# Optimization experiments

Measured on AMD Instinct MI355X. Metric: run time of the kernel, lower is better.

The kernel has to match this reference:

```python
import jax, jax.numpy as jnp
import numpy as np

LN_EPS = 1e-5
REG_STRENGTH = 0.01  # torchsort soft_rank regularization_strength


def layer_norm(x, g, b):
    mu = jnp.mean(x, axis=-1, keepdims=True)
    var = jnp.var(x, axis=-1, keepdims=True)
    return (x - mu) * jax.lax.rsqrt(var + LN_EPS) * g + b


def pava_blocks(y):
    """Block ids of the non-increasing isotonic regression of y (PAVA).
    Returns int32 [n]: index of the block each position belongs to."""
    n = y.shape[0]

    def step(carry, yi):
        sums, counts, size = carry
        sums = sums.at[size].set(yi)
        counts = counts.at[size].set(1)
        size = size + 1

        def cond(st):
            s_, c_, sz = st
            m_prev = s_[sz - 2] / jnp.maximum(c_[sz - 2], 1).astype(s_.dtype)
            m_top = s_[sz - 1] / jnp.maximum(c_[sz - 1], 1).astype(s_.dtype)
            return (sz >= 2) & (m_prev <= m_top)

        def body(st):
            s_, c_, sz = st
            s_ = s_.at[sz - 2].add(s_[sz - 1])
            c_ = c_.at[sz - 2].add(c_[sz - 1])
            return s_, c_, sz - 1

        sums, counts, size = jax.lax.while_loop(cond, body, (sums, counts, size))
        return (sums, counts, size), None

    init = (jnp.zeros(n, y.dtype), jnp.zeros(n, jnp.int32), jnp.int32(0))
    (sums, counts, size), _ = jax.lax.scan(step, init, y)
    # expand block index over positions; trailing counts are 0 so total == n
    return jnp.repeat(jnp.arange(n, dtype=jnp.int32), counts, total_repeat_length=n)


def isotonic_l2_noninc(y):
    """argmin_{v1>=v2>=...>=vn} ||v - y||^2 via PAVA; block structure is
    computed on stop_gradient(y), solution is a differentiable segment mean."""
    n = y.shape[0]
    bid = pava_blocks(jax.lax.stop_gradient(y))
    bsum = jax.ops.segment_sum(y, bid, num_segments=n)
    bcnt = jax.ops.segment_sum(jnp.ones_like(y), bid, num_segments=n)
    return (bsum / jnp.maximum(bcnt, 1.0))[bid]


def soft_rank_row(scores):
    """torchsort.soft_rank(regularization='l2') on one row [n]."""
    n = scores.shape[0]
    theta = scores / REG_STRENGTH
    perm = jax.lax.stop_gradient(jnp.argsort(-theta))  # descending sort perm
    s = theta[perm]
    w = jnp.arange(n, 0, -1, dtype=scores.dtype)  # [n, n-1, ..., 1]
    dual = isotonic_l2_noninc(s - w)
    primal = s - dual
    return jnp.zeros(n, scores.dtype).at[perm].set(primal)


def setup_inputs() -> dict:
    key = jax.random.key(0)
    ks = jax.random.split(key, 3)
    B, rows, feat, hid = 32, 16384, 256, 16
    return {
        "table": jax.random.normal(ks[0], (B, rows, feat), dtype=jnp.float32),
        "ln1_g": jnp.ones((feat,), jnp.float32),
        "ln1_b": jnp.zeros((feat,), jnp.float32),
        "W1": 0.02 * jax.random.normal(ks[1], (feat, hid), dtype=jnp.float32),
        "b1": jnp.zeros((hid,), jnp.float32),
        "ln2_g": jnp.ones((hid,), jnp.float32),
        "ln2_b": jnp.zeros((hid,), jnp.float32),
        "W2": 0.02 * jax.random.normal(ks[2], (hid, 1), dtype=jnp.float32),
        "b2": jnp.zeros((1,), jnp.float32),
        "capacity": 64,
    }


def reference(table, ln1_g, ln1_b, W1, b1, ln2_g, ln2_b, W2, b2, capacity):
    B, rows, feat = table.shape
    h = layer_norm(table, ln1_g, ln1_b)
    h = jax.nn.relu(jnp.einsum('brf,fh->brh', h, W1) + b1)
    h = layer_norm(h, ln2_g, ln2_b)
    scores = (jnp.einsum('brh,ho->bro', h, W2) + b2)[..., 0]  # [B, rows]
    mn = jnp.min(scores, axis=1, keepdims=True)
    mx = jnp.max(scores, axis=1, keepdims=True)
    scaled = (scores - mn) / (mx - mn) * 100.0
    soft_ranks = jax.vmap(soft_rank_row)(scaled)  # [B, rows]
    hard_ranks = jnp.argsort(jnp.argsort(scores, axis=1), axis=1)  # inverse perm
    bins = hard_ranks // capacity + 1
    return soft_ranks[..., None], bins[..., None]
```

## Files before the change

### kernel.cpp

```cpp
#include <hip/hip_runtime.h>

#define NB 32
#define NR 16384
#define NF 256
#define NH 16
#define TOT (NB*NR)
#define RPB 256
#define KC 32
#define LSTR 33
#define SEGP 16386

typedef unsigned long long u64;

__device__ __forceinline__ unsigned int f2u(float f) {
    unsigned int u = __float_as_uint(f);
    return (u & 0x80000000u) ? ~u : (u | 0x80000000u);
}
__device__ __forceinline__ float u2f(unsigned int s) {
    unsigned int u = (s & 0x80000000u) ? (s ^ 0x80000000u) : ~s;
    return __uint_as_float(u);
}

__global__ __launch_bounds__(256) void k_prep(
    const float* __restrict__ ln1_g, const float* __restrict__ ln1_b,
    const float* __restrict__ W1, const float* __restrict__ b1,
    const float* __restrict__ ln2_g, const float* __restrict__ ln2_b,
    const float* __restrict__ W2, const float* __restrict__ b2,
    float* __restrict__ W1g, float* __restrict__ consts,
    unsigned* __restrict__ mnmx)
{
    __shared__ float redc[16][16];
    __shared__ float redu[16][16];
    const int t = threadIdx.x;
    for (int e = t; e < NF*NH; e += 256) {
        int k = e >> 4;
        W1g[e] = ln1_g[k] * W1[e];
    }
    if (t < NB) { mnmx[2*t] = 0u; mnmx[2*t + 1] = 0xFFFFFFFFu; }
    const int h = t & 15, kp = t >> 4;
    float pc = 0.f, pu = 0.f;
    #pragma unroll
    for (int r = 0; r < 16; ++r) {
        int k = kp*16 + r;
        float w = W1[k*NH + h];
        pc += ln1_b[k] * w;
        pu += ln1_g[k] * w;
    }
    redc[kp][h] = pc; redu[kp][h] = pu;
    __syncthreads();
    if (t < 16) {
        float sc = 0.f, su = 0.f;
        #pragma unroll
        for (int r = 0; r < 16; ++r) { sc += redc[r][t]; su += redu[r][t]; }
        consts[t]      = sc + b1[t];
        consts[16 + t] = su;
        consts[32 + t] = ln2_g[t] * W2[t];
    }
    if (t == 0) {
        float U2 = 0.f, C2 = b2[0];
        for (int hh = 0; hh < 16; ++hh) {
            U2 += ln2_g[hh] * W2[hh];
            C2 += ln2_b[hh] * W2[hh];
        }
        consts[48] = U2;
        consts[49] = C2;
    }
}

__global__ __launch_bounds__(256) void k_scores(
    const float* __restrict__ table,
    const float* __restrict__ W1g,
    const float* __restrict__ consts,
    u64* __restrict__ keys, unsigned* __restrict__ mnmx)
{
    __shared__ float xt[RPB * LSTR];
    __shared__ unsigned redmx[4], redmn[4];
    const int t = threadIdx.x;
    const size_t rowBase = (size_t)blockIdx.x * RPB;
    const int bb = blockIdx.x >> 6;
    const float4* __restrict__ Wg4 = (const float4*)W1g;

    float dx[16];
    #pragma unroll
    for (int h = 0; h < 16; ++h) dx[h] = 0.f;
    float sum = 0.f, ssq = 0.f;

    for (int c = 0; c < NF/KC; ++c) {
        float4 v[8];
        #pragma unroll
        for (int p = 0; p < 8; ++p) {
            int q = p*256 + t;
            int r = q >> 3, cg = q & 7;
            v[p] = *(const float4*)(table + (rowBase + r)*NF + c*KC + cg*4);
        }
        __syncthreads();
        #pragma unroll
        for (int p = 0; p < 8; ++p) {
            int q = p*256 + t;
            int r = q >> 3, cg = q & 7;
            float* dst = xt + r*LSTR + cg*4;
            dst[0] = v[p].x; dst[1] = v[p].y; dst[2] = v[p].z; dst[3] = v[p].w;
        }
        __syncthreads();

        const float* __restrict__ xr = xt + t*LSTR;
        #pragma unroll 4
        for (int k = 0; k < KC; ++k) {
            const int kk = c*KC + k;
            float x = xr[k];
            float4 w0 = Wg4[kk*4+0];
            float4 w1 = Wg4[kk*4+1];
            float4 w2 = Wg4[kk*4+2];
            float4 w3 = Wg4[kk*4+3];
            sum += x;
            ssq = fmaf(x, x, ssq);
            dx[ 0] = fmaf(x, w0.x, dx[ 0]);
            dx[ 1] = fmaf(x, w0.y, dx[ 1]);
            dx[ 2] = fmaf(x, w0.z, dx[ 2]);
            dx[ 3] = fmaf(x, w0.w, dx[ 3]);
            dx[ 4] = fmaf(x, w1.x, dx[ 4]);
            dx[ 5] = fmaf(x, w1.y, dx[ 5]);
            dx[ 6] = fmaf(x, w1.z, dx[ 6]);
            dx[ 7] = fmaf(x, w1.w, dx[ 7]);
            dx[ 8] = fmaf(x, w2.x, dx[ 8]);
            dx[ 9] = fmaf(x, w2.y, dx[ 9]);
            dx[10] = fmaf(x, w2.z, dx[10]);
            dx[11] = fmaf(x, w2.w, dx[11]);
            dx[12] = fmaf(x, w3.x, dx[12]);
            dx[13] = fmaf(x, w3.y, dx[13]);
            dx[14] = fmaf(x, w3.z, dx[14]);
            dx[15] = fmaf(x, w3.w, dx[15]);
        }
    }

    const float mu   = sum * (1.f/NF);
    const float var  = ssq * (1.f/NF) - mu*mu;
    const float rstd = rsqrtf(var + 1e-5f);
    float s2 = 0.f, q2 = 0.f, dh = 0.f;
    #pragma unroll
    for (int h = 0; h < 16; ++h) {
        float hv = rstd * (dx[h] - mu * consts[16 + h]) + consts[h];
        hv = fmaxf(hv, 0.f);
        s2 += hv;
        q2 = fmaf(hv, hv, q2);
        dh = fmaf(hv, consts[32 + h], dh);
    }
    const float mu2   = s2 * (1.f/NH);
    const float var2  = q2 * (1.f/NH) - mu2*mu2;
    const float rstd2 = rsqrtf(var2 + 1e-5f);
    const float sc    = rstd2 * (dh - mu2 * consts[48]) + consts[49];

    const size_t row = rowBase + t;
    const unsigned k32 = f2u(sc);
    keys[row] = ((u64)k32 << 32) | (u64)(row & (NR-1));

    unsigned wmx = k32, wmn = k32;
    #pragma unroll
    for (int m = 32; m >= 1; m >>= 1) {
        wmx = max(wmx, (unsigned)__shfl_xor((int)wmx, m, 64));
        wmn = min(wmn, (unsigned)__shfl_xor((int)wmn, m, 64));
    }
    const int lane = t & 63, wid = t >> 6;
    if (lane == 0) { redmx[wid] = wmx; redmn[wid] = wmn; }
    __syncthreads();
    if (t == 0) {
        unsigned bx = redmx[0], bn = redmn[0];
        #pragma unroll
        for (int w = 1; w < 4; ++w) { bx = max(bx, redmx[w]); bn = min(bn, redmn[w]); }
        atomicMax(&mnmx[2*bb], bx);
        atomicMin(&mnmx[2*bb + 1], bn);
    }
}

__global__ __launch_bounds__(1024) void k_sort_local(u64* __restrict__ keys) {
    __shared__ u64 sk[4096];
    const int base_g = blockIdx.x * 4096;
    const int tid = threadIdx.x;
    #pragma unroll
    for (int it = 0; it < 4; ++it) sk[tid + it*1024] = keys[base_g + tid + it*1024];
    __syncthreads();
    for (int k = 2; k <= 4096; k <<= 1) {
        for (int j = k >> 1; j > 0; j >>= 1) {
            int ii[2]; u64 a[2], c[2];
            #pragma unroll
            for (int it = 0; it < 2; ++it) {
                int q = tid + it*1024;
                int i = ((q & ~(j-1)) << 1) | (q & (j-1));
                ii[it] = i;
                a[it] = sk[i]; c[it] = sk[i | j];
            }
            #pragma unroll
            for (int it = 0; it < 2; ++it) {
                int gi = (base_g + ii[it]) & (NR - 1);
                bool dir = ((gi & k) == 0);
                if ((c[it] > a[it]) == dir) { sk[ii[it]] = c[it]; sk[ii[it] | j] = a[it]; }
            }
            __syncthreads();
        }
    }
    #pragma unroll
    for (int it = 0; it < 4; ++it) keys[base_g + tid + it*1024] = sk[tid + it*1024];
}

__global__ __launch_bounds__(1024) void k_mtail(u64* __restrict__ keys, int K) {
    __shared__ u64 sk[4096];
    const int base_g = blockIdx.x * 4096;
    const int tid = threadIdx.x;
    #pragma unroll
    for (int it = 0; it < 4; ++it) sk[tid + it*1024] = keys[base_g + tid + it*1024];
    const bool dir = (((base_g & (NR-1)) & K) == 0);
    __syncthreads();
    for (int j = 2048; j >= 1; j >>= 1) {
        int ii[2]; u64 a[2], c[2];
        #pragma unroll
        for (int it = 0; it < 2; ++it) {
            int q = tid + it*1024;
            int i = ((q & ~(j-1)) << 1) | (q & (j-1));
            ii[it] = i;
            a[it] = sk[i]; c[it] = sk[i | j];
        }
        #pragma unroll
        for (int it = 0; it < 2; ++it) {
            if ((c[it] > a[it]) == dir) { sk[ii[it]] = c[it]; sk[ii[it] | j] = a[it]; }
        }
        __syncthreads();
    }
    #pragma unroll
    for (int it = 0; it < 4; ++it) keys[base_g + tid + it*1024] = sk[tid + it*1024];
}

__global__ __launch_bounds__(256) void k_gpass(u64* __restrict__ keys, int k, int j) {
    int gt = blockIdx.x * 256 + threadIdx.x;
    int b  = gt >> 13;
    int t  = gt & 8191;
    int i  = ((t & ~(j-1)) << 1) | (t & (j-1));
    bool dir = ((i & k) == 0);
    u64* kb = keys + (size_t)b * NR;
    u64 a = kb[i], c = kb[i | j];
    if ((c > a) == dir) { kb[i] = c; kb[i | j] = a; }
}

__global__ __launch_bounds__(1024) void k_hullA(
    u64* __restrict__ keys, const unsigned* __restrict__ mnmx,
    int* __restrict__ Hg, double* __restrict__ Svg,
    int* __restrict__ cntg, double* __restrict__ sumg)
{
    __shared__ __align__(16) char smem[32768 + 16384 + 128 + 1024 + 3*512];
    u64*    sk  = (u64*)smem;
    double* S   = (double*)smem;
    int*    H   = (int*)(smem + 32768);
    double* Wt  = (double*)(smem + 32768 + 16384);
    int*    cnt = (int*)(smem + 32768 + 16384 + 128);
    int*    ti  = (int*)(smem + 32768 + 16384 + 128 + 1024);
    int*    tj  = (int*)(smem + 32768 + 16384 + 128 + 1024 + 512);
    int*    crA = (int*)(smem + 32768 + 16384 + 128 + 1024 + 1024);

    const int blk = blockIdx.x;
    const int b = blk >> 2, c = blk & 3;
    const int tid = threadIdx.x, lane = tid & 63, wid = tid >> 6;
    u64* kg = keys + (size_t)b * NR + c * 4096;

    #pragma unroll
    for (int it = 0; it < 4; ++it) sk[tid + it*1024] = kg[tid + it*1024];
    __syncthreads();
    for (int j = 2048; j >= 1; j >>= 1) {
        int ii[2]; u64 a[2], cc[2];
        #pragma unroll
        for (int it = 0; it < 2; ++it) {
            int q = tid + it*1024;
            int i = ((q & ~(j-1)) << 1) | (q & (j-1));
            ii[it] = i;
            a[it] = sk[i]; cc[it] = sk[i | j];
        }
        #pragma unroll
        for (int it = 0; it < 2; ++it) {
            if (cc[it] > a[it]) { sk[ii[it]] = cc[it]; sk[ii[it] | j] = a[it]; }
        }
        __syncthreads();
    }

    const float mx = u2f(mnmx[2*b]);
    const float mn = u2f(mnmx[2*b + 1]);
    const float scale = 10000.0f / (mx - mn);
    const int gofs = c * 4096;
    const int b4 = tid * 4;

    u64 kv[4];
    #pragma unroll
    for (int r = 0; r < 4; ++r) kv[r] = sk[b4 + r];
    #pragma unroll
    for (int it = 0; it < 4; ++it) kg[tid + it*1024] = sk[tid + it*1024];

    double loc[4];
    double acc = 0.0;
    #pragma unroll
    for (int r = 0; r < 4; ++r) {
        int ig = gofs + b4 + r;
        float s_i = (u2f((unsigned)(kv[r] >> 32)) - mn) * scale;
        acc += (double)s_i - (double)(NR - ig);
        loc[r] = acc;
    }
    __syncthreads();

    double v = acc;
    #pragma unroll
    for (int d = 1; d < 64; d <<= 1) {
        double o = __shfl_up(v, d, 64);
        if (lane >= d) v += o;
    }
    if (lane == 63) Wt[wid] = v;
    __syncthreads();
    if (tid < 16) {
        double w = Wt[tid];
        #pragma unroll
        for (int d = 1; d < 16; d <<= 1) {
            double o = __shfl_up(w, d, 16);
            if ((tid & 15) >= d) w += o;
        }
        Wt[tid] = w;
    }
    __syncthreads();
    const double wbase = (wid == 0) ? 0.0 : Wt[wid - 1];
    const double excl = wbase + (v - acc);
    #pragma unroll
    for (int r = 0; r < 4; ++r) S[b4 + r] = excl + loc[r];
    __syncthreads();
    if (tid == 0) sumg[blk] = S[4095];

    #define SVA(k) ((k) == 0 ? 0.0 : S[(k)-1])

    if (tid < 256) {
        const int base16 = tid * 16;
        int out = 0;
        int k1 = 0, k2 = 0; double y1 = 0.0, y2 = 0.0;
        #pragma unroll 1
        for (int r = 0; r < 16; ++r) {
            int k = base16 + r;
            double yk = SVA(k);
            while (out >= 2) {
                double cr_ = (double)(k1 - k2)*(yk - y2) - (y1 - y2)*(double)(k - k2);
                if (cr_ >= 0.0) {
                    --out; k1 = k2; y1 = y2;
                    if (out >= 2) { k2 = H[base16 + out - 2]; y2 = SVA(k2); }
                } else break;
            }
            H[base16 + out] = k;
            k2 = k1; y2 = y1; k1 = k; y1 = yk;
            ++out;
        }
        cnt[tid] = out;
    }

    for (int lev = 0; lev < 8; ++lev) {
        __syncthreads();
        const int pairs = 128 >> lev;
        const int Wd = 16 << lev;
        if (tid < pairs) {
            const int lbase = tid * 2 * Wd;
            const int rbase = lbase + Wd;
            int cl = cnt[(2*tid) << lev];
            int cr = cnt[(2*tid+1) << lev];
            int i = cl - 1, j = 0;
            int kLi = H[lbase + i];            double yLi = SVA(kLi);
            int kLm = 0;                       double yLm = 0.0;
            if (i > 0) { kLm = H[lbase + i - 1]; yLm = SVA(kLm); }
            int kRj = H[rbase];                double yRj = SVA(kRj);
            int kRn = 0;                       double yRn = 0.0;
            if (cr > 1) { kRn = H[rbase + 1]; yRn = SVA(kRn); }
            bool moved = true;
            while (moved) {
                moved = false;
                while (i > 0) {
                    double cr_ = (double)(kLi - kLm)*(yRj - yLm)
                               - (yLi - yLm)*(double)(kRj - kLm);
                    if (cr_ >= 0.0) {
                        --i; kLi = kLm; yLi = yLm;
                        if (i > 0) { kLm = H[lbase + i - 1]; yLm = SVA(kLm); }
                        moved = true;
                    } else break;
                }
                while (j < cr - 1) {
                    double cr_ = (double)(kRj - kLi)*(yRn - yLi)
                               - (yRj - yLi)*(double)(kRn - kLi);
                    if (cr_ >= 0.0) {
                        ++j; kRj = kRn; yRj = yRn;
                        if (j < cr - 1) { kRn = H[rbase + j + 1]; yRn = SVA(kRn); }
                        moved = true;
                    } else break;
                }
            }
            ti[tid] = i; tj[tid] = j; crA[tid] = cr;
            cnt[(2*tid) << lev] = (i + 1) + (cr - j);
        }
        __syncthreads();
        const int tpp = 8 << lev;
        const int p = tid / tpp;
        const int q = tid % tpp;
        int vals[8];
        int len = 0, srcb = 0, dstb = 0;
        if (p < pairs) {
            const int lbase = p * 2 * Wd;
            const int rbase = lbase + Wd;
            const int i = ti[p], j = tj[p], cr = crA[p];
            len = cr - j;
            srcb = rbase + j;
            dstb = lbase + i + 1;
            #pragma unroll
            for (int t2 = 0; t2 < 8; ++t2) {
                int e2 = q + t2 * tpp;
                if (e2 < len) vals[t2] = H[srcb + e2];
            }
        }
        __syncthreads();
        if (p < pairs) {
            #pragma unroll
            for (int t2 = 0; t2 < 8; ++t2) {
                int e2 = q + t2 * tpp;
                if (e2 < len) H[dstb + e2] = vals[t2];
            }
        }
        __syncthreads();
    }

    const int m = cnt[0];
    for (int p = tid; p < m; p += 1024) {
        int k = H[p];
        Hg[(size_t)blk * 4096 + p]  = k + gofs;
        Svg[(size_t)blk * 4096 + p] = SVA(k);
    }
    if (tid == 0) cntg[blk] = m;
    #undef SVA
}

__global__ __launch_bounds__(1024) void k_hullB(
    const double* __restrict__ sumg,
    int* __restrict__ Hg, double* __restrict__ Svg,
    const int* __restrict__ cntg,
    int* __restrict__ segk, float* __restrict__ segs, int* __restrict__ mseg)
{
    __shared__ int cnt[4];
    __shared__ int tiS[2], tjS[2], crS[2];
    __shared__ double beta[5];
    const int b = blockIdx.x;
    const int tid = threadIdx.x;
    int*    Hb = Hg  + (size_t)b * NR;
    double* Sb = Svg + (size_t)b * NR;

    if (tid < 4) cnt[tid] = cntg[4*b + tid];
    if (tid == 0) {
        double s = 0.0;
        #pragma unroll
        for (int c = 0; c < 4; ++c) { beta[c] = s; s += sumg[4*b + c]; }
        beta[4] = s;
    }
    __syncthreads();

    #pragma unroll 1
    for (int c = 0; c < 4; ++c) {
        const double bc = beta[c];
        for (int p = tid; p < cnt[c]; p += 1024) Sb[c*4096 + p] += bc;
    }
    __syncthreads();

    for (int lev = 0; lev < 2; ++lev) {
        const int pairs = 2 >> lev;
        const int Wd = 4096 << lev;
        if (tid < pairs) {
            const int lbase = tid * 2 * Wd;
            const int rbase = lbase + Wd;
            int cl = cnt[(2*tid) << lev];
            int cr = cnt[(2*tid+1) << lev];
            int i = cl - 1, j = 0;
            int kLi = Hb[lbase + i];            double yLi = Sb[lbase + i];
            int kLm = 0;                        double yLm = 0.0;
            if (i > 0) { kLm = Hb[lbase + i - 1]; yLm = Sb[lbase + i - 1]; }
            int kRj = Hb[rbase];                double yRj = Sb[rbase];
            int kRn = 0;                        double yRn = 0.0;
            if (cr > 1) { kRn = Hb[rbase + 1]; yRn = Sb[rbase + 1]; }
            bool moved = true;
            while (moved) {
                moved = false;
                while (i > 0) {
                    double cr_ = (double)(kLi - kLm)*(yRj - yLm)
                               - (yLi - yLm)*(double)(kRj - kLm);
                    if (cr_ >= 0.0) {
                        --i; kLi = kLm; yLi = yLm;
                        if (i > 0) { kLm = Hb[lbase + i - 1]; yLm = Sb[lbase + i - 1]; }
                        moved = true;
                    } else break;
                }
                while (j < cr - 1) {
                    double cr_ = (double)(kRj - kLi)*(yRn - yLi)
                               - (yRj - yLi)*(double)(kRn - kLi);
                    if (cr_ >= 0.0) {
                        ++j; kRj = kRn; yRj = yRn;
                        if (j < cr - 1) { kRn = Hb[rbase + j + 1]; yRn = Sb[rbase + j + 1]; }
                        moved = true;
                    } else break;
                }
            }
            tiS[tid] = i; tjS[tid] = j; crS[tid] = cr;
            cnt[(2*tid) << lev] = (i + 1) + (cr - j);
        }
        __syncthreads();
        const int tpp = (lev == 0) ? 512 : 1024;
        const int p = tid / tpp;
        const int q = tid % tpp;
        int hv[8]; double sv[8];
        int len = 0, srcb = 0, dstb = 0;
        if (p < pairs) {
            const int lbase = p * 2 * Wd;
            const int rbase = lbase + Wd;
            const int i = tiS[p], j = tjS[p], cr = crS[p];
            len = cr - j;
            srcb = rbase + j;
            dstb = lbase + i + 1;
            #pragma unroll
            for (int t2 = 0; t2 < 8; ++t2) {
                int e2 = q + t2 * tpp;
                if (e2 < len) { hv[t2] = Hb[srcb + e2]; sv[t2] = Sb[srcb + e2]; }
            }
        }
        __syncthreads();
        if (p < pairs) {
            #pragma unroll
            for (int t2 = 0; t2 < 8; ++t2) {
                int e2 = q + t2 * tpp;
                if (e2 < len) { Hb[dstb + e2] = hv[t2]; Sb[dstb + e2] = sv[t2]; }
            }
        }
        __syncthreads();
    }

    if (tid == 0) {
        const double total = beta[4];
        int out = cnt[0];
        while (out >= 2) {
            int ka = Hb[out - 2], kb2 = Hb[out - 1];
            double ya = Sb[out - 2], yb = Sb[out - 1];
            double cr_ = (double)(kb2 - ka)*(total - ya) - (yb - ya)*(double)(NR - ka);
            if (cr_ >= 0.0) --out;
            else break;
        }
        Hb[out] = NR; Sb[out] = total;
        cnt[0] = out + 1;
    }
    __syncthreads();

    const int m = cnt[0];
    for (int p = tid; p < m - 1; p += 1024) {
        int ka = Hb[p], kb2 = Hb[p + 1];
        segk[(size_t)b * SEGP + p] = ka;
        segs[(size_t)b * SEGP + p] = (float)((Sb[p + 1] - Sb[p]) / (double)(kb2 - ka));
    }
    if (tid == 0) mseg[b] = m;
}

__global__ __launch_bounds__(256) void k_out(
    const u64* __restrict__ keys, const unsigned* __restrict__ mnmx,
    const int* __restrict__ capp,
    const int* __restrict__ segk, const float* __restrict__ segs,
    const int* __restrict__ mseg,
    float* __restrict__ out_soft, float* __restrict__ out_bins)
{
    const int gb = blockIdx.x;
    const int b = gb >> 4, part = gb & 15;
    const int tid = threadIdx.x;
    const int m = mseg[b];
    const float mx = u2f(mnmx[2*b]);
    const float mn = u2f(mnmx[2*b + 1]);
    const float scale = 10000.0f / (mx - mn);
    const int cap = capp[0];
    const int base = part * 1024;
    const int* __restrict__ sk2 = segk + (size_t)b * SEGP;
    const float* __restrict__ ss2 = segs + (size_t)b * SEGP;

    int lo[4], hi[4];
    #pragma unroll
    for (int r = 0; r < 4; ++r) { lo[r] = 0; hi[r] = m - 1; }
    for (int step = 0; step < 14; ++step) {
        int hm[4];
        #pragma unroll
        for (int r = 0; r < 4; ++r)
            if (hi[r] - lo[r] > 1) hm[r] = sk2[(lo[r] + hi[r]) >> 1];
        #pragma unroll
        for (int r = 0; r < 4; ++r) {
            if (hi[r] - lo[r] > 1) {
                int mid = (lo[r] + hi[r]) >> 1;
                int i = base + tid + (r << 8);
                if (hm[r] <= i) lo[r] = mid; else hi[r] = mid;
            }
        }
    }
    #pragma unroll
    for (int r = 0; r < 4; ++r) {
        const int i = base + tid + (r << 8);
        u64 key = keys[(size_t)b * NR + i];
        float s_i = (u2f((unsigned)(key >> 32)) - mn) * scale;
        float primal = s_i - ss2[lo[r]];
        int idx = (int)(key & 0xffffffffu);
        out_soft[(size_t)b * NR + idx] = primal;
        int rank = (NR - 1) - i;
        out_bins[(size_t)b * NR + idx] = (float)(rank / cap + 1);
    }
}

extern "C" void kernel_launch(void* const* d_in, const int* in_sizes, int n_in,
                              void* d_out, int out_size, void* d_ws, size_t ws_size,
                              hipStream_t stream)
{
    const float* table = (const float*)d_in[0];
    const float* ln1_g = (const float*)d_in[1];
    const float* ln1_b = (const float*)d_in[2];
    const float* W1    = (const float*)d_in[3];
    const float* b1    = (const float*)d_in[4];
    const float* ln2_g = (const float*)d_in[5];
    const float* ln2_b = (const float*)d_in[6];
    const float* W2    = (const float*)d_in[7];
    const float* b2    = (const float*)d_in[8];
    const int*   cap   = (const int*)d_in[9];

    u64*      keys   = (u64*)d_ws;
    double*   Svg    = (double*)(keys + TOT);
    double*   sumg   = Svg + TOT;
    float*    W1g    = (float*)(sumg + 128);
    float*    consts = W1g + NF*NH;
    unsigned* mnmx   = (unsigned*)(consts + 64);
    int*      Hg     = (int*)(mnmx + 64);
    int*      cntg   = Hg + TOT;
    int*      segk   = cntg + 128;
    float*    segs   = (float*)(segk + NB*SEGP);
    int*      mseg   = (int*)(segs + NB*SEGP);

    float* out_soft = (float*)d_out;
    float* out_bins = ((float*)d_out) + TOT;

    k_prep<<<1, 256, 0, stream>>>(ln1_g, ln1_b, W1, b1, ln2_g, ln2_b, W2, b2,
                                  W1g, consts, mnmx);
    k_scores<<<TOT/RPB, 256, 0, stream>>>(table, W1g, consts, keys, mnmx);

    k_sort_local<<<TOT/4096, 1024, 0, stream>>>(keys);
    k_gpass<<<TOT/512, 256, 0, stream>>>(keys, 8192, 4096);
    k_mtail<<<TOT/4096, 1024, 0, stream>>>(keys, 8192);
    k_gpass<<<TOT/512, 256, 0, stream>>>(keys, 16384, 8192);
    k_gpass<<<TOT/512, 256, 0, stream>>>(keys, 16384, 4096);

    k_hullA<<<NB*4, 1024, 0, stream>>>(keys, mnmx, Hg, Svg, cntg, sumg);
    k_hullB<<<NB, 1024, 0, stream>>>(sumg, Hg, Svg, cntg, segk, segs, mseg);
    k_out<<<NB*16, 256, 0, stream>>>(keys, mnmx, cap, segk, segs, mseg,
                                     out_soft, out_bins);
}
```

Baseline: 305.4 us.

## Restructure bitonic merge stages and fuse hull merge with output via last-block atomic

```diff
diff --git a/kernel.cpp b/kernel.cpp
--- a/kernel.cpp
+++ b/kernel.cpp
@@ -8,7 +8,6 @@
 #define RPB 256
 #define KC 32
 #define LSTR 33
-#define SEGP 16386
 
 typedef unsigned long long u64;
 
@@ -27,7 +26,7 @@
     const float* __restrict__ ln2_g, const float* __restrict__ ln2_b,
     const float* __restrict__ W2, const float* __restrict__ b2,
     float* __restrict__ W1g, float* __restrict__ consts,
-    unsigned* __restrict__ mnmx)
+    unsigned* __restrict__ mnmx, unsigned* __restrict__ done)
 {
     __shared__ float redc[16][16];
     __shared__ float redu[16][16];
@@ -36,7 +35,7 @@
         int k = e >> 4;
         W1g[e] = ln1_g[k] * W1[e];
     }
-    if (t < NB) { mnmx[2*t] = 0u; mnmx[2*t + 1] = 0xFFFFFFFFu; }
+    if (t < NB) { mnmx[2*t] = 0u; mnmx[2*t + 1] = 0xFFFFFFFFu; done[t] = 0u; }
     const int h = t & 15, kp = t >> 4;
     float pc = 0.f, pu = 0.f;
     #pragma unroll
@@ -202,48 +201,54 @@
     for (int it = 0; it < 4; ++it) keys[base_g + tid + it*1024] = sk[tid + it*1024];
 }
 
-__global__ __launch_bounds__(1024) void k_mtail(u64* __restrict__ keys, int K) {
-    __shared__ u64 sk[4096];
-    const int base_g = blockIdx.x * 4096;
+__global__ __launch_bounds__(1024) void k_mid8(u64* __restrict__ keys) {
+    __shared__ u64 sk[8192];
+    const int base_g = blockIdx.x * 8192;
     const int tid = threadIdx.x;
     #pragma unroll
-    for (int it = 0; it < 4; ++it) sk[tid + it*1024] = keys[base_g + tid + it*1024];
-    const bool dir = (((base_g & (NR-1)) & K) == 0);
-    __syncthreads();
-    for (int j = 2048; j >= 1; j >>= 1) {
-        int ii[2]; u64 a[2], c[2];
-        #pragma unroll
-        for (int it = 0; it < 2; ++it) {
+    for (int it = 0; it < 8; ++it) sk[tid + it*1024] = keys[base_g + tid + it*1024];
+    const bool dir = (((base_g & (NR-1)) & 8192) == 0);
+    __syncthreads();
+    for (int j = 4096; j >= 1; j >>= 1) {
+        int ii[4]; u64 a[4], c[4];
+        #pragma unroll
+        for (int it = 0; it < 4; ++it) {
             int q = tid + it*1024;
             int i = ((q & ~(j-1)) << 1) | (q & (j-1));
             ii[it] = i;
             a[it] = sk[i]; c[it] = sk[i | j];
         }
         #pragma unroll
-        for (int it = 0; it < 2; ++it) {
+        for (int it = 0; it < 4; ++it) {
             if ((c[it] > a[it]) == dir) { sk[ii[it]] = c[it]; sk[ii[it] | j] = a[it]; }
         }
         __syncthreads();
     }
     #pragma unroll
-    for (int it = 0; it < 4; ++it) keys[base_g + tid + it*1024] = sk[tid + it*1024];
-}
-
-__global__ __launch_bounds__(256) void k_gpass(u64* __restrict__ keys, int k, int j) {
-    int gt = blockIdx.x * 256 + threadIdx.x;
-    int b  = gt >> 13;
-    int t  = gt & 8191;
-    int i  = ((t & ~(j-1)) << 1) | (t & (j-1));
-    bool dir = ((i & k) == 0);
-    u64* kb = keys + (size_t)b * NR;
-    u64 a = kb[i], c = kb[i | j];
-    if ((c > a) == dir) { kb[i] = c; kb[i | j] = a; }
-}
-
-__global__ __launch_bounds__(1024) void k_hullA(
+    for (int it = 0; it < 8; ++it) keys[base_g + tid + it*1024] = sk[tid + it*1024];
+}
+
+__global__ __launch_bounds__(256) void k_cross16(u64* __restrict__ keys) {
+    const int gt = blockIdx.x * 256 + threadIdx.x;
+    const int b = gt >> 12;
+    const int c = gt & 4095;
+    u64* kb = keys + (size_t)b * NR + c;
+    u64 e0 = kb[0], e1 = kb[4096], e2 = kb[8192], e3 = kb[12288];
+    u64 t;
+    if (e2 > e0) { t = e0; e0 = e2; e2 = t; }
+    if (e3 > e1) { t = e1; e1 = e3; e3 = t; }
+    if (e1 > e0) { t = e0; e0 = e1; e1 = t; }
+    if (e3 > e2) { t = e2; e2 = e3; e3 = t; }
+    kb[0] = e0; kb[4096] = e1; kb[8192] = e2; kb[12288] = e3;
+}
+
+__global__ __launch_bounds__(1024) void k_hullAB(
     u64* __restrict__ keys, const unsigned* __restrict__ mnmx,
+    const int* __restrict__ capp,
     int* __restrict__ Hg, double* __restrict__ Svg,
-    int* __restrict__ cntg, double* __restrict__ sumg)
+    int* __restrict__ cntg, double* __restrict__ sumg,
+    unsigned* __restrict__ done,
+    float* __restrict__ out_soft, float* __restrict__ out_bins)
 {
     __shared__ __align__(16) char smem[32768 + 16384 + 128 + 1024 + 3*512];
     u64*    sk  = (u64*)smem;
@@ -254,6 +259,10 @@
     int*    ti  = (int*)(smem + 32768 + 16384 + 128 + 1024);
     int*    tj  = (int*)(smem + 32768 + 16384 + 128 + 1024 + 512);
     int*    crA = (int*)(smem + 32768 + 16384 + 128 + 1024 + 1024);
+    __shared__ double beta[5];
+    __shared__ int cntB[4];
+    __shared__ int tiS[2], tjS[2], crS[2];
+    __shared__ int amLast;
 
     const int blk = blockIdx.x;
     const int b = blk >> 2, c = blk & 3;
@@ -422,43 +431,41 @@
         __syncthreads();
     }
 
-    const int m = cnt[0];
-    for (int p = tid; p < m; p += 1024) {
+    const int m0 = cnt[0];
+    for (int p = tid; p < m0; p += 1024) {
         int k = H[p];
         Hg[(size_t)blk * 4096 + p]  = k + gofs;
         Svg[(size_t)blk * 4096 + p] = SVA(k);
     }
-    if (tid == 0) cntg[blk] = m;
+    if (tid == 0) cntg[blk] = m0;
     #undef SVA
-}
-
-__global__ __launch_bounds__(1024) void k_hullB(
-    const double* __restrict__ sumg,
-    int* __restrict__ Hg, double* __restrict__ Svg,
-    const int* __restrict__ cntg,
-    int* __restrict__ segk, float* __restrict__ segs, int* __restrict__ mseg)
-{
-    __shared__ int cnt[4];
-    __shared__ int tiS[2], tjS[2], crS[2];
-    __shared__ double beta[5];
-    const int b = blockIdx.x;
-    const int tid = threadIdx.x;
+    __syncthreads();
+
+    if (tid == 0) {
+        __threadfence();
+        unsigned old = atomicAdd(&done[b], 1u);
+        amLast = (old == 3u);
+    }
+    __syncthreads();
+    if (!amLast) return;
+    __threadfence();
+
     int*    Hb = Hg  + (size_t)b * NR;
     double* Sb = Svg + (size_t)b * NR;
 
-    if (tid < 4) cnt[tid] = cntg[4*b + tid];
+    if (tid < 4) cntB[tid] = cntg[4*b + tid];
     if (tid == 0) {
         double s = 0.0;
         #pragma unroll
-        for (int c = 0; c < 4; ++c) { beta[c] = s; s += sumg[4*b + c]; }
+        for (int cc = 0; cc < 4; ++cc) { beta[cc] = s; s += sumg[4*b + cc]; }
         beta[4] = s;
     }
     __syncthreads();
 
     #pragma unroll 1
-    for (int c = 0; c < 4; ++c) {
-        const double bc = beta[c];
-        for (int p = tid; p < cnt[c]; p += 1024) Sb[c*4096 + p] += bc;
+    for (int cc = 0; cc < 4; ++cc) {
+        const double bc = beta[cc];
+        for (int p = tid; p < cntB[cc]; p += 1024) Sb[cc*4096 + p] += bc;
     }
     __syncthreads();
 
@@ -468,8 +475,8 @@
         if (tid < pairs) {
             const int lbase = tid * 2 * Wd;
             const int rbase = lbase + Wd;
-            int cl = cnt[(2*tid) << lev];
-            int cr = cnt[(2*tid+1) << lev];
+            int cl = cntB[(2*tid) << lev];
+            int cr = cntB[(2*tid+1) << lev];
             int i = cl - 1, j = 0;
             int kLi = Hb[lbase + i];            double yLi = Sb[lbase + i];
             int kLm = 0;                        double yLm = 0.0;
@@ -500,7 +507,7 @@
                 }
             }
             tiS[tid] = i; tjS[tid] = j; crS[tid] = cr;
-            cnt[(2*tid) << lev] = (i + 1) + (cr - j);
+            cntB[(2*tid) << lev] = (i + 1) + (cr - j);
         }
         __syncthreads();
         const int tpp = (lev == 0) ? 512 : 1024;
@@ -534,7 +541,7 @@
 
     if (tid == 0) {
         const double total = beta[4];
-        int out = cnt[0];
+        int out = cntB[0];
         while (out >= 2) {
             int ka = Hb[out - 2], kb2 = Hb[out - 1];
             double ya = Sb[out - 2], yb = Sb[out - 1];
@@ -543,61 +550,38 @@
             else break;
         }
         Hb[out] = NR; Sb[out] = total;
-        cnt[0] = out + 1;
-    }
-    __syncthreads();
-
-    const int m = cnt[0];
-    for (int p = tid; p < m - 1; p += 1024) {
-        int ka = Hb[p], kb2 = Hb[p + 1];
-        segk[(size_t)b * SEGP + p] = ka;
-        segs[(size_t)b * SEGP + p] = (float)((Sb[p + 1] - Sb[p]) / (double)(kb2 - ka));
-    }
-    if (tid == 0) mseg[b] = m;
-}
-
-__global__ __launch_bounds__(256) void k_out(
-    const u64* __restrict__ keys, const unsigned* __restrict__ mnmx,
-    const int* __restrict__ capp,
-    const int* __restrict__ segk, const float* __restrict__ segs,
-    const int* __restrict__ mseg,
-    float* __restrict__ out_soft, float* __restrict__ out_bins)
-{
-    const int gb = blockIdx.x;
-    const int b = gb >> 4, part = gb & 15;
-    const int tid = threadIdx.x;
-    const int m = mseg[b];
-    const float mx = u2f(mnmx[2*b]);
-    const float mn = u2f(mnmx[2*b + 1]);
-    const float scale = 10000.0f / (mx - mn);
+        cntB[0] = out + 1;
+    }
+    __syncthreads();
+
+    const int m = cntB[0];
     const int cap = capp[0];
-    const int base = part * 1024;
-    const int* __restrict__ sk2 = segk + (size_t)b * SEGP;
-    const float* __restrict__ ss2 = segs + (size_t)b * SEGP;
-
-    int lo[4], hi[4];
-    #pragma unroll
-    for (int r = 0; r < 4; ++r) { lo[r] = 0; hi[r] = m - 1; }
-    for (int step = 0; step < 14; ++step) {
-        int hm[4];
-        #pragma unroll
-        for (int r = 0; r < 4; ++r)
-            if (hi[r] - lo[r] > 1) hm[r] = sk2[(lo[r] + hi[r]) >> 1];
-        #pragma unroll
-        for (int r = 0; r < 4; ++r) {
-            if (hi[r] - lo[r] > 1) {
-                int mid = (lo[r] + hi[r]) >> 1;
-                int i = base + tid + (r << 8);
-                if (hm[r] <= i) lo[r] = mid; else hi[r] = mid;
-            }
-        }
-    }
-    #pragma unroll
-    for (int r = 0; r < 4; ++r) {
-        const int i = base + tid + (r << 8);
-        u64 key = keys[(size_t)b * NR + i];
+    const u64* kbat = keys + (size_t)b * NR;
+    int lo_[16], hi_[16];
+    #pragma unroll
+    for (int r = 0; r < 16; ++r) { lo_[r] = 0; hi_[r] = m - 1; }
+    for (int step = 0; step < 15; ++step) {
+        int hm[16];
+        #pragma unroll
+        for (int r = 0; r < 16; ++r)
+            if (hi_[r] - lo_[r] > 1) hm[r] = Hb[(lo_[r] + hi_[r]) >> 1];
+        #pragma unroll
+        for (int r = 0; r < 16; ++r) {
+            if (hi_[r] - lo_[r] > 1) {
+                int mid = (lo_[r] + hi_[r]) >> 1;
+                int i = tid + (r << 10);
+                if (hm[r] <= i) lo_[r] = mid; else hi_[r] = mid;
+            }
+        }
+    }
+    #pragma unroll 1
+    for (int r = 0; r < 16; ++r) {
+        const int i = tid + (r << 10);
+        int ka = Hb[lo_[r]], kb2 = Hb[lo_[r] + 1];
+        double slope = (Sb[lo_[r] + 1] - Sb[lo_[r]]) / (double)(kb2 - ka);
+        u64 key = kbat[i];
         float s_i = (u2f((unsigned)(key >> 32)) - mn) * scale;
-        float primal = s_i - ss2[lo[r]];
+        float primal = (float)((double)s_i - slope);
         int idx = (int)(key & 0xffffffffu);
         out_soft[(size_t)b * NR + idx] = primal;
         int rank = (NR - 1) - i;
@@ -626,27 +610,19 @@
     float*    W1g    = (float*)(sumg + 128);
     float*    consts = W1g + NF*NH;
     unsigned* mnmx   = (unsigned*)(consts + 64);
-    int*      Hg     = (int*)(mnmx + 64);
+    unsigned* done   = mnmx + 64;
+    int*      Hg     = (int*)(done + 32);
     int*      cntg   = Hg + TOT;
-    int*      segk   = cntg + 128;
-    float*    segs   = (float*)(segk + NB*SEGP);
-    int*      mseg   = (int*)(segs + NB*SEGP);
 
     float* out_soft = (float*)d_out;
     float* out_bins = ((float*)d_out) + TOT;
 
     k_prep<<<1, 256, 0, stream>>>(ln1_g, ln1_b, W1, b1, ln2_g, ln2_b, W2, b2,
-                                  W1g, consts, mnmx);
+                                  W1g, consts, mnmx, done);
     k_scores<<<TOT/RPB, 256, 0, stream>>>(table, W1g, consts, keys, mnmx);
-
     k_sort_local<<<TOT/4096, 1024, 0, stream>>>(keys);
-    k_gpass<<<TOT/512, 256, 0, stream>>>(keys, 8192, 4096);
-    k_mtail<<<TOT/4096, 1024, 0, stream>>>(keys, 8192);
-    k_gpass<<<TOT/512, 256, 0, stream>>>(keys, 16384, 8192);
-    k_gpass<<<TOT/512, 256, 0, stream>>>(keys, 16384, 4096);
-
-    k_hullA<<<NB*4, 1024, 0, stream>>>(keys, mnmx, Hg, Svg, cntg, sumg);
-    k_hullB<<<NB, 1024, 0, stream>>>(sumg, Hg, Svg, cntg, segk, segs, mseg);
-    k_out<<<NB*16, 256, 0, stream>>>(keys, mnmx, cap, segk, segs, mseg,
-                                     out_soft, out_bins);
-}
+    k_mid8<<<TOT/8192, 1024, 0, stream>>>(keys);
+    k_cross16<<<TOT/1024, 256, 0, stream>>>(keys);
+    k_hullAB<<<NB*4, 1024, 0, stream>>>(keys, mnmx, cap, Hg, Svg, cntg, sumg,
+                                        done, out_soft, out_bins);
+}
```

After: 344.6 us. +12.9%, slower.
